# Kernel tuning notes

Hardware: AMD Instinct MI355X
Metric: run time of the kernel (lower is better)

The kernel has to match this reference:

```python
import jax, jax.numpy as jnp
import numpy as np


def _resize_bilinear(x, h, w):
    # matches F.upsample(mode='bilinear', align_corners=False) (half-pixel centers)
    return jax.image.resize(x, (x.shape[0], x.shape[1], h, w), method='bilinear')


def _build_volume_2d(fl, fr, maxdisp):
    # fl, fr: [B,C,H,W] -> cost [B,D,H,W], D=maxdisp (stride=1)
    B, C, H, W = fl.shape
    d = jnp.arange(maxdisp)
    src = jnp.arange(W)[None, :] - d[:, None]          # [D,W]
    valid = (src >= 0).astype(fl.dtype)
    src_c = jnp.clip(src, 0, W - 1)
    fr_sh = fr[:, :, :, src_c] * valid                  # [B,C,H,D,W]; zeros where w<d
    cost = jnp.abs(fl[:, :, :, None, :] - fr_sh).sum(axis=1)  # [B,H,D,W]
    return jnp.transpose(cost, (0, 2, 1, 3))            # [B,D,H,W]


def _warp(fr, disp):
    # fr: [B,C,H,W]; disp: [B,K,H,W] horizontal disparity (sample at x - disp)
    # bilinear along W, zero padding (grid_sample semantics, align_corners=True grid)
    B, C, H, W = fr.shape
    xs = jnp.arange(W, dtype=fr.dtype)[None, None, None, :] - disp   # [B,K,H,W]
    x0 = jnp.floor(xs)
    w1 = xs - x0                                        # frac weight for right neighbor
    x0i = x0.astype(jnp.int32)
    x1i = x0i + 1
    v0 = ((x0i >= 0) & (x0i < W)).astype(fr.dtype)
    v1 = ((x1i >= 0) & (x1i < W)).astype(fr.dtype)
    x0c = jnp.clip(x0i, 0, W - 1)
    x1c = jnp.clip(x1i, 0, W - 1)

    def gather(idx):  # idx [B,K,H,W] -> [B,K,C,H,W]
        idxb = jnp.broadcast_to(idx[:, :, None, :, :], (B, idx.shape[1], C, H, W))
        return jnp.take_along_axis(fr[:, None], idxb, axis=-1)

    g0 = gather(x0c) * v0[:, :, None]
    g1 = gather(x1c) * v1[:, :, None]
    return g0 * (1.0 - w1)[:, :, None] + g1 * w1[:, :, None]   # [B,K,C,H,W]


def _build_volume_2d3(fl, fr, maxdisp, disp):
    # fl, fr: [B,C,H,W]; disp: [B,1,H,W] coarse disparity. K = 2*maxdisp-1 shifts.
    shifts = jnp.arange(-maxdisp + 1, maxdisp, dtype=fl.dtype)       # [K]
    bd = disp - shifts[None, :, None, None]                          # [B,K,H,W]
    warped = _warp(fr, bd)                                           # [B,K,C,H,W]
    return jnp.abs(fl[:, None] - warped).sum(axis=2)                 # [B,K,H,W]


def _regress(cost, start, end):
    # softmax(-cost) over disparity axis, weighted sum with disp values [start,end)
    p = jax.nn.softmax(-cost, axis=1)
    dvals = jnp.arange(start, end, dtype=cost.dtype)[None, :, None, None]
    return jnp.sum(p * dvals, axis=1, keepdims=True)                 # [B,1,H,W]


def setup_inputs() -> dict:
    key = jax.random.key(0)
    k = jax.random.split(key, 4)
    return {
        "feat_l0": jax.random.normal(k[0], (4, 32, 64, 128), dtype=jnp.float32),
        "feat_r0": jax.random.normal(k[1], (4, 32, 64, 128), dtype=jnp.float32),
        "feat_l1": jax.random.normal(k[2], (4, 32, 128, 256), dtype=jnp.float32),
        "feat_r1": jax.random.normal(k[3], (4, 32, 128, 256), dtype=jnp.float32),
        "img_h": 512,
        "img_w": 1024,
        "maxdisp0": 12,
        "maxdisp1": 3,
    }


def reference(feat_l0, feat_r0, feat_l1, feat_r1, img_h, img_w, maxdisp0, maxdisp1):
    H0 = feat_l0.shape[2]
    H1, W1 = feat_l1.shape[2], feat_l1.shape[3]

    cost0 = _build_volume_2d(feat_l0, feat_r0, maxdisp0)             # [B,D0,H0,W0]
    pred_low0 = _regress(cost0, 0, maxdisp0) * (img_h / H0)
    pred0 = _resize_bilinear(pred_low0, img_h, img_w)                # [B,1,img_h,img_w]

    # ---- scale 1: residual cost volume via warp around coarse disparity ----
    wflow = _resize_bilinear(pred0, H1, W1) * (H1 / img_h)           # [B,1,H1,W1]
    cost1 = _build_volume_2d3(feat_l1, feat_r1, maxdisp1, wflow)     # [B,2*D1-1,H1,W1]
    pred_low1 = _regress(cost1, -maxdisp1 + 1, maxdisp1) * (img_h / H1)
    pred1 = _resize_bilinear(pred_low1, img_h, img_w) + pred0

    return (pred0, pred1)
```

## Files before the change

kernel.cpp:

```cpp
#include <hip/hip_runtime.h>

#define NB 4
#define NC 32
#define H0 64
#define W0 128
#define D0 12
#define H1 128
#define W1 256
#define NK 5
#define IMH 512
#define IMW 1024

__device__ __forceinline__ float bilin(const float* __restrict__ img, int H, int W,
                                       float sy, float sx) {
    float y0f = floorf(sy), x0f = floorf(sx);
    float fy = sy - y0f, fx = sx - x0f;
    int y0 = (int)y0f, x0 = (int)x0f;
    int y0c = min(max(y0, 0), H - 1);
    int y1c = min(max(y0 + 1, 0), H - 1);
    int x0c = min(max(x0, 0), W - 1);
    int x1c = min(max(x0 + 1, 0), W - 1);
    float v00 = img[y0c * W + x0c];
    float v01 = img[y0c * W + x1c];
    float v10 = img[y1c * W + x0c];
    float v11 = img[y1c * W + x1c];
    float a = v00 * (1.f - fx) + v01 * fx;
    float b = v10 * (1.f - fx) + v11 * fx;
    return a * (1.f - fy) + b * fy;
}

__global__ __launch_bounds__(512) void k_cost0(const float* __restrict__ fl,
                                               const float* __restrict__ fr,
                                               float* __restrict__ pl0) {
    const int bh = blockIdx.x;
    const int b = bh >> 6, h = bh & (H0 - 1);
    const int tid = threadIdx.x;
    __shared__ float frs[NC][W0];
    __shared__ float part[4][D0][W0];

    const size_t rowbase = ((size_t)b * NC * H0 + h) * W0;

#pragma unroll
    for (int i = 0; i < 2; ++i) {
        int f4 = i * 512 + tid;
        int c = f4 >> 5, w4 = f4 & 31;
        ((float4*)frs)[f4] =
            *(const float4*)(fr + rowbase + (size_t)c * (H0 * W0) + w4 * 4);
    }
    __syncthreads();

    const int g = tid >> 7, w = tid & (W0 - 1);
    float cost[D0];
#pragma unroll
    for (int d = 0; d < D0; ++d) cost[d] = 0.f;
#pragma unroll
    for (int j = 0; j < 8; ++j) {
        int c = g * 8 + j;
        float flv = fl[rowbase + (size_t)c * (H0 * W0) + w];
#pragma unroll
        for (int d = 0; d < D0; ++d) {
            float rv = (w >= d) ? frs[c][w - d] : 0.f;
            cost[d] += fabsf(flv - rv);
        }
    }
#pragma unroll
    for (int d = 0; d < D0; ++d) part[g][d][w] = cost[d];
    __syncthreads();

    if (tid < W0) {
        float tc[D0];
#pragma unroll
        for (int d = 0; d < D0; ++d)
            tc[d] = part[0][d][tid] + part[1][d][tid] + part[2][d][tid] + part[3][d][tid];
        float m = tc[0];
#pragma unroll
        for (int d = 1; d < D0; ++d) m = fminf(m, tc[d]);
        float s = 0.f, sd = 0.f;
#pragma unroll
        for (int d = 0; d < D0; ++d) {
            float e = expf(m - tc[d]);
            s += e;
            sd += (float)d * e;
        }
        pl0[(size_t)bh * W0 + tid] = 8.f * (sd / s);
    }
}

__global__ __launch_bounds__(512) void k_cost1(const float* __restrict__ fl,
                                               const float* __restrict__ fr,
                                               const float* __restrict__ pl0,
                                               float* __restrict__ pl1) {
    const int bh = blockIdx.x;
    const int b = bh >> 7, oy = bh & (H1 - 1);
    const int tid = threadIdx.x;
    __shared__ float frs[NC][W1];
    __shared__ float part[2][NK][W1];
    __shared__ float ytmp[W0];
    __shared__ float wfl[W1];

    const size_t rowbase = ((size_t)b * NC * H1 + oy) * W1;

    if (tid < W0) {
        const float* p0b = pl0 + (size_t)b * H0 * W0;
        int m = oy >> 1;
        int r0, r1, r2;
        float wy0, wy1, wy2;
        if (oy == 0) {
            r0 = 0; r1 = 0; r2 = 1;
            wy0 = 0.f; wy1 = 27.625f / 28.f; wy2 = 0.375f / 28.f;
        } else if (oy == H1 - 1) {
            r0 = H0 - 2; r1 = H0 - 1; r2 = H0 - 1;
            wy0 = 0.375f / 28.f; wy1 = 27.625f / 28.f; wy2 = 0.f;
        } else {
            r0 = max(m - 1, 0); r1 = m; r2 = min(m + 1, H0 - 1);
            if (oy & 1) { wy0 = 0.375f / 32.f; wy1 = 23.25f / 32.f; wy2 = 8.375f / 32.f; }
            else        { wy0 = 8.375f / 32.f; wy1 = 23.25f / 32.f; wy2 = 0.375f / 32.f; }
        }
        ytmp[tid] = wy0 * p0b[r0 * W0 + tid] + wy1 * p0b[r1 * W0 + tid]
                  + wy2 * p0b[r2 * W0 + tid];
    }

#pragma unroll
    for (int i = 0; i < 4; ++i) {
        int f4 = i * 512 + tid;
        int c = f4 >> 6, w4 = f4 & 63;
        ((float4*)frs)[f4] =
            *(const float4*)(fr + rowbase + (size_t)c * (H1 * W1) + w4 * 4);
    }
    __syncthreads();

    if (tid < W1) {
        int ox = tid, n = ox >> 1;
        int c0, c1, c2;
        float wx0, wx1, wx2;
        if (ox == 0) {
            c0 = 0; c1 = 0; c2 = 1;
            wx0 = 0.f; wx1 = 27.625f / 28.f; wx2 = 0.375f / 28.f;
        } else if (ox == W1 - 1) {
            c0 = W0 - 2; c1 = W0 - 1; c2 = W0 - 1;
            wx0 = 0.375f / 28.f; wx1 = 27.625f / 28.f; wx2 = 0.f;
        } else {
            c0 = max(n - 1, 0); c1 = n; c2 = min(n + 1, W0 - 1);
            if (ox & 1) { wx0 = 0.375f / 32.f; wx1 = 23.25f / 32.f; wx2 = 8.375f / 32.f; }
            else        { wx0 = 8.375f / 32.f; wx1 = 23.25f / 32.f; wx2 = 0.375f / 32.f; }
        }
        wfl[ox] = 0.25f * (wx0 * ytmp[c0] + wx1 * ytmp[c1] + wx2 * ytmp[c2]);
    }
    __syncthreads();

    const int half = tid >> 8, w = tid & (W1 - 1);
    float disp = wfl[w];
    int xi0[NK];
    float frw[NK];
#pragma unroll
    for (int k = 0; k < NK; ++k) {
        float xs = (float)w - disp + (float)(k - 2);
        float x0f = floorf(xs);
        frw[k] = xs - x0f;
        xi0[k] = (int)x0f;
    }
    float cost[NK];
#pragma unroll
    for (int k = 0; k < NK; ++k) cost[k] = 0.f;
#pragma unroll
    for (int j = 0; j < 16; ++j) {
        int c = half * 16 + j;
        float flv = fl[rowbase + (size_t)c * (H1 * W1) + w];
#pragma unroll
        for (int k = 0; k < NK; ++k) {
            int x0 = xi0[k], x1 = x0 + 1;
            float g0 = (x0 >= 0 && x0 < W1) ? frs[c][x0] : 0.f;
            float g1 = (x1 >= 0 && x1 < W1) ? frs[c][x1] : 0.f;
            cost[k] += fabsf(flv - (g0 * (1.f - frw[k]) + g1 * frw[k]));
        }
    }
#pragma unroll
    for (int k = 0; k < NK; ++k) part[half][k][w] = cost[k];
    __syncthreads();

    if (tid < W1) {
        float tc[NK];
#pragma unroll
        for (int k = 0; k < NK; ++k) tc[k] = part[0][k][tid] + part[1][k][tid];
        float m = tc[0];
#pragma unroll
        for (int k = 1; k < NK; ++k) m = fminf(m, tc[k]);
        float s = 0.f, sd = 0.f;
#pragma unroll
        for (int k = 0; k < NK; ++k) {
            float e = expf(m - tc[k]);
            s += e;
            sd += (float)(k - 2) * e;
        }
        pl1[(size_t)bh * W1 + tid] = 4.f * (sd / s);
    }
}

__global__ void k_final(const float* __restrict__ pl0, const float* __restrict__ pl1,
                        float* __restrict__ out) {
    const int NPX = NB * IMH * IMW;
    int t = blockIdx.x * blockDim.x + threadIdx.x;
    if (t >= NPX / 4) return;
    int xq = t & (IMW / 4 - 1);
    int tmp = t >> 8;
    int y = tmp & (IMH - 1);
    int b = tmp >> 9;

    const float* p0b = pl0 + (size_t)b * H0 * W0;
    const float* p1b = pl1 + (size_t)b * H1 * W1;
    float sy0 = (y + 0.5f) * 0.125f - 0.5f;
    float sy1 = (y + 0.5f) * 0.25f - 0.5f;

    float v0[4], v1[4];
#pragma unroll
    for (int i = 0; i < 4; ++i) {
        int x = xq * 4 + i;
        float sx0 = (x + 0.5f) * 0.125f - 0.5f;
        float sx1 = (x + 0.5f) * 0.25f - 0.5f;
        float p0 = bilin(p0b, H0, W0, sy0, sx0);
        v0[i] = p0;
        v1[i] = bilin(p1b, H1, W1, sy1, sx1) + p0;
    }
    ((float4*)out)[t] = make_float4(v0[0], v0[1], v0[2], v0[3]);
    ((float4*)(out + NPX))[t] = make_float4(v1[0], v1[1], v1[2], v1[3]);
}

extern "C" void kernel_launch(void* const* d_in, const int* in_sizes, int n_in,
                              void* d_out, int out_size, void* d_ws, size_t ws_size,
                              hipStream_t stream) {
    const float* fl0 = (const float*)d_in[0];
    const float* fr0 = (const float*)d_in[1];
    const float* fl1 = (const float*)d_in[2];
    const float* fr1 = (const float*)d_in[3];
    float* out = (float*)d_out;

    float* ws = (float*)d_ws;
    float* pred_low0 = ws;
    float* pred_low1 = ws + 32768;

    k_cost0<<<NB * H0, 512, 0, stream>>>(fl0, fr0, pred_low0);
    k_cost1<<<NB * H1, 512, 0, stream>>>(fl1, fr1, pred_low0, pred_low1);

    int n4 = NB * IMH * IMW / 4;
    k_final<<<(n4 + 255) / 256, 256, 0, stream>>>(pred_low0, pred_low1, out);
}
```

Baseline: 28.45 us.

## Restructure cost kernels: lane-split channel reduction, guard-padded LDS, async global-to-LDS loads

k_cost0 now splits each row across two blocks and assigns 8 lanes per pixel with a channel split. The channel reduction uses wave shuffles instead of a shared-memory partial buffer and an extra barrier. Both kernels store the right feature row in LDS with zero guard columns, which removes the per-tap bounds checks. k_cost1 loads the row through global_load_lds and shares six neighbour taps across the five shifts. The risks are the correctness of the guard sizing and the async LDS load, which is consumed after only a __syncthreads, plus extra shuffle cost.

```diff
diff --git a/kernel.cpp b/kernel.cpp
--- a/kernel.cpp
+++ b/kernel.cpp
@@ -10,6 +10,14 @@
 #define NK 5
 #define IMH 512
 #define IMW 1024
+
+#define FR0_STRIDE 84
+#define FR0_GUARD  16
+#define FR1_STRIDE 288
+#define FR1_GUARD  28
+
+typedef __attribute__((address_space(3))) uint32_t as3_u32;
+typedef const __attribute__((address_space(1))) uint32_t as1_u32;
 
 __device__ __forceinline__ float bilin(const float* __restrict__ img, int H, int W,
                                        float sy, float sx) {
@@ -32,57 +40,61 @@
 __global__ __launch_bounds__(512) void k_cost0(const float* __restrict__ fl,
                                                const float* __restrict__ fr,
                                                float* __restrict__ pl0) {
-    const int bh = blockIdx.x;
-    const int b = bh >> 6, h = bh & (H0 - 1);
+    const int blk = blockIdx.x;
+    const int row = blk >> 1;
+    const int half = blk & 1;
+    const int w0 = half * 64;
+    const int b = row >> 6, h = row & (H0 - 1);
     const int tid = threadIdx.x;
-    __shared__ float frs[NC][W0];
-    __shared__ float part[4][D0][W0];
+    __shared__ float frs[NC][FR0_STRIDE];
 
     const size_t rowbase = ((size_t)b * NC * H0 + h) * W0;
 
 #pragma unroll
     for (int i = 0; i < 2; ++i) {
-        int f4 = i * 512 + tid;
-        int c = f4 >> 5, w4 = f4 & 31;
-        ((float4*)frs)[f4] =
-            *(const float4*)(fr + rowbase + (size_t)c * (H0 * W0) + w4 * 4);
+        int idx = i * 512 + tid;
+        if (idx < NC * 20) {
+            int c = idx / 20, q = idx - c * 20;
+            int colg = w0 - 16 + q * 4;
+            float4 v = make_float4(0.f, 0.f, 0.f, 0.f);
+            if (colg >= 0)
+                v = *(const float4*)(fr + rowbase + (size_t)c * (H0 * W0) + colg);
+            *(float4*)&frs[c][q * 4] = v;
+        }
     }
     __syncthreads();
 
-    const int g = tid >> 7, w = tid & (W0 - 1);
+    const int wloc = tid >> 3, g = tid & 7;
     float cost[D0];
 #pragma unroll
     for (int d = 0; d < D0; ++d) cost[d] = 0.f;
 #pragma unroll
-    for (int j = 0; j < 8; ++j) {
-        int c = g * 8 + j;
-        float flv = fl[rowbase + (size_t)c * (H0 * W0) + w];
+    for (int j = 0; j < 4; ++j) {
+        int c = g + 8 * j;
+        float flv = fl[rowbase + (size_t)c * (H0 * W0) + w0 + wloc];
+        const float* sr = &frs[c][FR0_GUARD + wloc];
+#pragma unroll
+        for (int d = 0; d < D0; ++d)
+            cost[d] += fabsf(flv - sr[-d]);
+    }
+#pragma unroll
+    for (int d = 0; d < D0; ++d) {
+        cost[d] += __shfl_xor(cost[d], 1);
+        cost[d] += __shfl_xor(cost[d], 2);
+        cost[d] += __shfl_xor(cost[d], 4);
+    }
+    if (g == 0) {
+        float m = cost[0];
+#pragma unroll
+        for (int d = 1; d < D0; ++d) m = fminf(m, cost[d]);
+        float s = 0.f, sd = 0.f;
 #pragma unroll
         for (int d = 0; d < D0; ++d) {
-            float rv = (w >= d) ? frs[c][w - d] : 0.f;
-            cost[d] += fabsf(flv - rv);
-        }
-    }
-#pragma unroll
-    for (int d = 0; d < D0; ++d) part[g][d][w] = cost[d];
-    __syncthreads();
-
-    if (tid < W0) {
-        float tc[D0];
-#pragma unroll
-        for (int d = 0; d < D0; ++d)
-            tc[d] = part[0][d][tid] + part[1][d][tid] + part[2][d][tid] + part[3][d][tid];
-        float m = tc[0];
-#pragma unroll
-        for (int d = 1; d < D0; ++d) m = fminf(m, tc[d]);
-        float s = 0.f, sd = 0.f;
-#pragma unroll
-        for (int d = 0; d < D0; ++d) {
-            float e = expf(m - tc[d]);
+            float e = expf(m - cost[d]);
             s += e;
             sd += (float)d * e;
         }
-        pl0[(size_t)bh * W0 + tid] = 8.f * (sd / s);
+        pl0[(size_t)row * W0 + w0 + wloc] = 8.f * (sd / s);
     }
 }
 
@@ -90,15 +102,33 @@
                                                const float* __restrict__ fr,
                                                const float* __restrict__ pl0,
                                                float* __restrict__ pl1) {
-    const int bh = blockIdx.x;
-    const int b = bh >> 7, oy = bh & (H1 - 1);
+    const int blk = blockIdx.x;
+    const int b = blk >> 7, oy = blk & (H1 - 1);
     const int tid = threadIdx.x;
-    __shared__ float frs[NC][W1];
-    __shared__ float part[2][NK][W1];
+    __shared__ float frs1p[NC][FR1_STRIDE];
     __shared__ float ytmp[W0];
     __shared__ float wfl[W1];
 
-    const size_t rowbase = ((size_t)b * NC * H1 + oy) * W1;
+    const size_t rowbase1 = ((size_t)b * NC * H1 + oy) * W1;
+
+    {
+        const int wave = tid >> 6, lane = tid & 63;
+#pragma unroll
+        for (int j = 0; j < 4; ++j) {
+            int c = wave * 4 + j;
+            const float* src = fr + rowbase1 + (size_t)c * (H1 * W1) + lane * 4;
+            as3_u32* dst = (as3_u32*)(&frs1p[c][FR1_GUARD]);
+            __builtin_amdgcn_global_load_lds((as1_u32*)src, dst, 16, 0, 0);
+        }
+    }
+
+#pragma unroll
+    for (int i = 0; i < 2; ++i) {
+        int idx = i * 512 + tid;
+        int r = idx >> 5, q = idx & 31;
+        int col = (q < FR1_GUARD) ? q : (FR1_GUARD + W1 + (q - FR1_GUARD));
+        frs1p[r][col] = 0.f;
+    }
 
     if (tid < W0) {
         const float* p0b = pl0 + (size_t)b * H0 * W0;
@@ -119,14 +149,6 @@
         ytmp[tid] = wy0 * p0b[r0 * W0 + tid] + wy1 * p0b[r1 * W0 + tid]
                   + wy2 * p0b[r2 * W0 + tid];
     }
-
-#pragma unroll
-    for (int i = 0; i < 4; ++i) {
-        int f4 = i * 512 + tid;
-        int c = f4 >> 6, w4 = f4 & 63;
-        ((float4*)frs)[f4] =
-            *(const float4*)(fr + rowbase + (size_t)c * (H1 * W1) + w4 * 4);
-    }
     __syncthreads();
 
     if (tid < W1) {
@@ -148,51 +170,46 @@
     }
     __syncthreads();
 
-    const int half = tid >> 8, w = tid & (W1 - 1);
-    float disp = wfl[w];
-    int xi0[NK];
-    float frw[NK];
-#pragma unroll
-    for (int k = 0; k < NK; ++k) {
-        float xs = (float)w - disp + (float)(k - 2);
-        float x0f = floorf(xs);
-        frw[k] = xs - x0f;
-        xi0[k] = (int)x0f;
-    }
-    float cost[NK];
-#pragma unroll
-    for (int k = 0; k < NK; ++k) cost[k] = 0.f;
-#pragma unroll
-    for (int j = 0; j < 16; ++j) {
-        int c = half * 16 + j;
-        float flv = fl[rowbase + (size_t)c * (H1 * W1) + w];
-#pragma unroll
-        for (int k = 0; k < NK; ++k) {
-            int x0 = xi0[k], x1 = x0 + 1;
-            float g0 = (x0 >= 0 && x0 < W1) ? frs[c][x0] : 0.f;
-            float g1 = (x1 >= 0 && x1 < W1) ? frs[c][x1] : 0.f;
-            cost[k] += fabsf(flv - (g0 * (1.f - frw[k]) + g1 * frw[k]));
-        }
-    }
-#pragma unroll
-    for (int k = 0; k < NK; ++k) part[half][k][w] = cost[k];
-    __syncthreads();
-
-    if (tid < W1) {
-        float tc[NK];
-#pragma unroll
-        for (int k = 0; k < NK; ++k) tc[k] = part[0][k][tid] + part[1][k][tid];
-        float m = tc[0];
-#pragma unroll
-        for (int k = 1; k < NK; ++k) m = fminf(m, tc[k]);
-        float s = 0.f, sd = 0.f;
-#pragma unroll
-        for (int k = 0; k < NK; ++k) {
-            float e = expf(m - tc[k]);
-            s += e;
-            sd += (float)(k - 2) * e;
-        }
-        pl1[(size_t)bh * W1 + tid] = 4.f * (sd / s);
+    {
+        const int w = tid >> 1, h = tid & 1;
+        float disp = wfl[w];
+        float xs = (float)w - disp;
+        float xbf = floorf(xs);
+        float f = xs - xbf;
+        int xb = (int)xbf;
+        const float* sr = &frs1p[0][FR1_GUARD + xb - 2];
+
+        float cost[NK];
+#pragma unroll
+        for (int k = 0; k < NK; ++k) cost[k] = 0.f;
+#pragma unroll
+        for (int j = 0; j < 16; ++j) {
+            int c = 2 * j + h;
+            float flv = fl[rowbase1 + (size_t)c * (H1 * W1) + w];
+            const float* row = sr + c * FR1_STRIDE;
+            float g0 = row[0], g1 = row[1], g2 = row[2];
+            float g3 = row[3], g4 = row[4], g5 = row[5];
+            cost[0] += fabsf(flv - (g0 + f * (g1 - g0)));
+            cost[1] += fabsf(flv - (g1 + f * (g2 - g1)));
+            cost[2] += fabsf(flv - (g2 + f * (g3 - g2)));
+            cost[3] += fabsf(flv - (g3 + f * (g4 - g3)));
+            cost[4] += fabsf(flv - (g4 + f * (g5 - g4)));
+        }
+#pragma unroll
+        for (int k = 0; k < NK; ++k) cost[k] += __shfl_xor(cost[k], 1);
+        if (h == 0) {
+            float m = cost[0];
+#pragma unroll
+            for (int k = 1; k < NK; ++k) m = fminf(m, cost[k]);
+            float s = 0.f, sd = 0.f;
+#pragma unroll
+            for (int k = 0; k < NK; ++k) {
+                float e = expf(m - cost[k]);
+                s += e;
+                sd += (float)(k - 2) * e;
+            }
+            pl1[(size_t)blk * W1 + w] = 4.f * (sd / s);
+        }
     }
 }
 
@@ -235,12 +252,12 @@
     float* out = (float*)d_out;
 
     float* ws = (float*)d_ws;
-    float* pred_low0 = ws;
-    float* pred_low1 = ws + 32768;
-
-    k_cost0<<<NB * H0, 512, 0, stream>>>(fl0, fr0, pred_low0);
-    k_cost1<<<NB * H1, 512, 0, stream>>>(fl1, fr1, pred_low0, pred_low1);
+    float* pl0 = ws;
+    float* pl1 = ws + 32768;
+
+    k_cost0<<<NB * H0 * 2, 512, 0, stream>>>(fl0, fr0, pl0);
+    k_cost1<<<NB * H1, 512, 0, stream>>>(fl1, fr1, pl0, pl1);
 
     int n4 = NB * IMH * IMW / 4;
-    k_final<<<(n4 + 255) / 256, 256, 0, stream>>>(pred_low0, pred_low1, out);
-}
+    k_final<<<(n4 + 255) / 256, 256, 0, stream>>>(pl0, pl1, out);
+}
```

Result: faster. 26.62 us (-6.4%).
